# Kernel tuning notes

Measured on AMD Instinct MI355X. Metric: run time of the kernel, lower is better.

The kernel has to match this reference:

```python
import jax, jax.numpy as jnp
import numpy as np

B, L, D = 32, 8192, 256
M = L // 2 + 1  # max possible valley count (strict local minima can't be adjacent)


def setup_inputs() -> dict:
    key = jax.random.key(0)
    k1, k2, k3 = jax.random.split(key, 3)
    xs_pad = jax.random.normal(k1, (B, L, D), dtype=jnp.float32)
    olens = jax.random.randint(k2, (B,), 1, L + 1, dtype=jnp.int32)
    # linear_sigmoid params: Linear(256, 1)
    W = jax.random.normal(k3, (D, 1), dtype=jnp.float32) * 0.05
    b = jnp.zeros((1,), dtype=jnp.float32)
    return {"xs_pad": xs_pad, "olens": olens, "W": W, "b": b}


def reference(xs_pad, olens, W, b):
    Bq, Lq, Dq = xs_pad.shape
    # scalar importance: sigmoid(Linear(x))  [B, L, 1]
    s = jax.nn.sigmoid(xs_pad @ W + b)
    alpha_h = s * xs_pad                       # [B, L, D]
    sq = s[..., 0]                             # [B, L]
    # shifted neighbors, zero-padded at the ends (matches F.pad of the detached scalars)
    s_before = jnp.pad(sq[:, :-1], ((0, 0), (1, 0)))
    s_after = jnp.pad(sq[:, 1:], ((0, 0), (0, 1)))
    mask = (sq < s_before) & (sq < s_after)    # strict local minima
    mask = mask.at[:, 0].set(True)             # first frame forced to be a valley start
    counts = mask.sum(axis=1).astype(jnp.int32)  # per-batch valley count (returned olens)

    # valley starts, sorted, padded with sentinel L  -> [B, M]
    pos = jnp.arange(Lq)
    starts = jnp.sort(jnp.where(mask, pos, Lq), axis=1)[:, :M]
    valid = (starts < Lq)
    # segment = [start, min(start+2, L)) i.e. frames start and start+1 (clipped)
    i0 = jnp.clip(starts, 0, Lq - 1)
    i1 = jnp.clip(starts + 1, 0, Lq - 1)
    w0 = valid.astype(xs_pad.dtype)[..., None]
    w1 = ((starts + 1 < Lq) & valid).astype(xs_pad.dtype)[..., None]

    def gather(a, idx):
        return jnp.take_along_axis(a, idx[:, :, None], axis=1)

    num = gather(alpha_h, i0) * w0 + gather(alpha_h, i1) * w1   # [B, M, D]
    den = gather(s, i0) * w0 + gather(s, i1) * w1               # [B, M, 1]
    out = num / jnp.maximum(den, 1e-6)
    return out, counts
```

## Files before the change

### kernel.cpp

```cpp
#include <hip/hip_runtime.h>
#include <math.h>

#define B_ 32
#define L_ 8192
#define D_ 256
#define M_ 4097

__global__ __launch_bounds__(256) void k_sigmoid_dot(
    const float* __restrict__ x, const float* __restrict__ W,
    const float* __restrict__ bias, float* __restrict__ s)
{
    int row  = (blockIdx.x << 2) + (threadIdx.x >> 6);
    int lane = threadIdx.x & 63;
    const float4 xv = ((const float4*)(x + (size_t)row * D_))[lane];
    const float4 wv = ((const float4*)W)[lane];
    float p = xv.x * wv.x + xv.y * wv.y + xv.z * wv.z + xv.w * wv.w;
#pragma unroll
    for (int off = 32; off > 0; off >>= 1)
        p += __shfl_xor(p, off, 64);
    if (lane == 0) {
        float z = p + bias[0];
        s[row] = 1.0f / (1.0f + expf(-z));
    }
}

__global__ __launch_bounds__(256) void k_scan(
    const float* __restrict__ s, int* __restrict__ starts,
    int* __restrict__ counts, float* __restrict__ out_counts)
{
    int b = blockIdx.x;
    const float* sb = s + (size_t)b * L_;
    int t    = threadIdx.x;
    int base = t * 32;

    unsigned bits = 0;
    int cnt = 0;
    float sprev = (base == 0) ? 0.0f : sb[base - 1];
    float sc    = sb[base];
#pragma unroll 1
    for (int i = 0; i < 32; i++) {
        int l = base + i;
        float snext = (l == L_ - 1) ? 0.0f : sb[l + 1];
        bool m = (l == 0) ? true : ((sc < sprev) && (sc < snext));
        if (m) { bits |= (1u << i); cnt++; }
        sprev = sc;
        sc    = snext;
    }

    __shared__ int sh[256];
    sh[t] = cnt;
    __syncthreads();
    for (int off = 1; off < 256; off <<= 1) {
        int v = (t >= off) ? sh[t - off] : 0;
        __syncthreads();
        sh[t] += v;
        __syncthreads();
    }
    int excl  = sh[t] - cnt;
    int total = sh[255];

    int k = excl;
    for (int i = 0; i < 32; i++) {
        if (bits & (1u << i)) { starts[b * M_ + k] = base + i; k++; }
    }
    if (t == 0) {
        counts[b]     = total;
        out_counts[b] = (float)total;
    }
}

__global__ __launch_bounds__(64) void k_write(
    const float* __restrict__ x, const float* __restrict__ s,
    const int* __restrict__ starts, const int* __restrict__ counts,
    float* __restrict__ out)
{
    int k    = blockIdx.x;
    int b    = blockIdx.y;
    int lane = threadIdx.x;
    float4* orow = (float4*)(out + ((size_t)b * M_ + k) * D_);
    if (k >= counts[b]) {
        orow[lane] = make_float4(0.f, 0.f, 0.f, 0.f);
        return;
    }
    int p = starts[b * M_ + k];
    const float* sb = s + (size_t)b * L_;
    float s0 = sb[p];
    bool has1 = (p + 1 < L_);
    float s1 = has1 ? sb[p + 1] : 0.0f;
    float inv = 1.0f / fmaxf(s0 + s1, 1e-6f);

    const float4* x0 = (const float4*)(x + ((size_t)b * L_ + p) * D_);
    float4 a = x0[lane];
    float4 r;
    r.x = s0 * a.x; r.y = s0 * a.y; r.z = s0 * a.z; r.w = s0 * a.w;
    if (has1) {
        float4 c = (x0 + (D_ / 4))[lane];
        r.x += s1 * c.x; r.y += s1 * c.y; r.z += s1 * c.z; r.w += s1 * c.w;
    }
    r.x *= inv; r.y *= inv; r.z *= inv; r.w *= inv;
    orow[lane] = r;
}

extern "C" void kernel_launch(void* const* d_in, const int* in_sizes, int n_in,
                              void* d_out, int out_size, void* d_ws, size_t ws_size,
                              hipStream_t stream) {
    const float* x    = (const float*)d_in[0];
    const float* W    = (const float*)d_in[2];
    const float* bias = (const float*)d_in[3];

    float* out        = (float*)d_out;
    float* out_counts = out + (size_t)B_ * M_ * D_;

    float* s      = (float*)d_ws;
    int*   starts = (int*)((char*)d_ws + (size_t)B_ * L_ * 4);
    int*   counts = (int*)((char*)starts + (size_t)B_ * M_ * 4);

    k_sigmoid_dot<<<(B_ * L_) / 4, 256, 0, stream>>>(x, W, bias, s);
    k_scan<<<B_, 256, 0, stream>>>(s, starts, counts, out_counts);
    k_write<<<dim3(M_, B_), 64, 0, stream>>>(x, s, starts, counts, out);
}
```

Baseline: 422.5 us.

## Precompute valley weights in scan and widen write kernel blocks

The scan kernel now loads its 32-frame chunk with vectorized float4 reads, replaces the shared-memory block scan with a wave shuffle scan plus per-wave sums, and emits per-valley records holding the normalized weights and position. The write kernel reads one record per row instead of gathering s twice and dividing. It also processes 8 rows per 256-thread block instead of one row per 64-thread block, which cuts the launch grid size. The second x row load is now unconditional, using a clamped pointer. The workspace grows because records are float4 instead of int.

```diff
diff --git a/kernel.cpp b/kernel.cpp
--- a/kernel.cpp
+++ b/kernel.cpp
@@ -25,43 +25,71 @@
 }
 
 __global__ __launch_bounds__(256) void k_scan(
-    const float* __restrict__ s, int* __restrict__ starts,
+    const float* __restrict__ s, float4* __restrict__ rec,
     int* __restrict__ counts, float* __restrict__ out_counts)
 {
     int b = blockIdx.x;
     const float* sb = s + (size_t)b * L_;
     int t    = threadIdx.x;
+    int wid  = t >> 6;
+    int lane = t & 63;
     int base = t * 32;
+
+    float vals[34];
+    vals[0]  = (base == 0) ? 0.0f : sb[base - 1];
+    const float4* sb4 = (const float4*)(sb + base);
+#pragma unroll
+    for (int j = 0; j < 8; j++) {
+        float4 q = sb4[j];
+        vals[1 + 4 * j] = q.x; vals[2 + 4 * j] = q.y;
+        vals[3 + 4 * j] = q.z; vals[4 + 4 * j] = q.w;
+    }
+    vals[33] = (base + 32 >= L_) ? 0.0f : sb[base + 32];
 
     unsigned bits = 0;
     int cnt = 0;
-    float sprev = (base == 0) ? 0.0f : sb[base - 1];
-    float sc    = sb[base];
-#pragma unroll 1
+#pragma unroll
     for (int i = 0; i < 32; i++) {
-        int l = base + i;
-        float snext = (l == L_ - 1) ? 0.0f : sb[l + 1];
-        bool m = (l == 0) ? true : ((sc < sprev) && (sc < snext));
+        bool m = (base + i == 0)
+                 ? true
+                 : ((vals[i + 1] < vals[i]) && (vals[i + 1] < vals[i + 2]));
         if (m) { bits |= (1u << i); cnt++; }
-        sprev = sc;
-        sc    = snext;
     }
 
-    __shared__ int sh[256];
-    sh[t] = cnt;
+    int v = cnt;
+#pragma unroll
+    for (int off = 1; off < 64; off <<= 1) {
+        int u = __shfl_up(v, off, 64);
+        if (lane >= off) v += u;
+    }
+    __shared__ int wsum[4];
+    if (lane == 63) wsum[wid] = v;
     __syncthreads();
-    for (int off = 1; off < 256; off <<= 1) {
-        int v = (t >= off) ? sh[t - off] : 0;
-        __syncthreads();
-        sh[t] += v;
-        __syncthreads();
-    }
-    int excl  = sh[t] - cnt;
-    int total = sh[255];
+    int wo = 0;
+#pragma unroll
+    for (int w = 0; w < 4; w++)
+        if (w < wid) wo += wsum[w];
+    int excl  = v + wo - cnt;
+    int total = wsum[0] + wsum[1] + wsum[2] + wsum[3];
 
     int k = excl;
+#pragma unroll
     for (int i = 0; i < 32; i++) {
-        if (bits & (1u << i)) { starts[b * M_ + k] = base + i; k++; }
+        if (bits & (1u << i)) {
+            if (k < M_) {
+                int   p  = base + i;
+                float s0 = vals[i + 1];
+                float s1 = vals[i + 2];
+                float inv = 1.0f / fmaxf(s0 + s1, 1e-6f);
+                float4 r;
+                r.x = s0 * inv;
+                r.y = s1 * inv;
+                r.z = __int_as_float(p);
+                r.w = 0.0f;
+                rec[(size_t)b * M_ + k] = r;
+            }
+            k++;
+        }
     }
     if (t == 0) {
         counts[b]     = total;
@@ -69,36 +97,40 @@
     }
 }
 
-__global__ __launch_bounds__(64) void k_write(
-    const float* __restrict__ x, const float* __restrict__ s,
-    const int* __restrict__ starts, const int* __restrict__ counts,
-    float* __restrict__ out)
+__global__ __launch_bounds__(256) void k_write(
+    const float* __restrict__ x, const float4* __restrict__ rec,
+    const int* __restrict__ counts, float* __restrict__ out)
 {
-    int k    = blockIdx.x;
     int b    = blockIdx.y;
-    int lane = threadIdx.x;
-    float4* orow = (float4*)(out + ((size_t)b * M_ + k) * D_);
-    if (k >= counts[b]) {
-        orow[lane] = make_float4(0.f, 0.f, 0.f, 0.f);
-        return;
+    int wid  = threadIdx.x >> 6;
+    int lane = threadIdx.x & 63;
+    int cnt  = counts[b];
+    if (cnt > M_) cnt = M_;
+    int kb   = blockIdx.x * 8 + wid;
+#pragma unroll
+    for (int rr = 0; rr < 2; rr++) {
+        int k = kb + (rr << 2);
+        if (k >= M_) continue;
+        float4* orow = (float4*)(out + ((size_t)b * M_ + k) * D_);
+        if (k >= cnt) {
+            orow[lane] = make_float4(0.f, 0.f, 0.f, 0.f);
+            continue;
+        }
+        float4 r4 = rec[(size_t)b * M_ + k];
+        int p = __float_as_int(r4.z);
+        if (p < 0) p = 0;
+        if (p > L_ - 1) p = L_ - 1;
+        const float4* xp = (const float4*)(x + ((size_t)b * L_ + p) * D_);
+        float4 a = xp[lane];
+        const float4* xq = xp + ((p + 1 < L_) ? (D_ / 4) : 0);
+        float4 c = xq[lane];
+        float4 r;
+        r.x = r4.x * a.x + r4.y * c.x;
+        r.y = r4.x * a.y + r4.y * c.y;
+        r.z = r4.x * a.z + r4.y * c.z;
+        r.w = r4.x * a.w + r4.y * c.w;
+        orow[lane] = r;
     }
-    int p = starts[b * M_ + k];
-    const float* sb = s + (size_t)b * L_;
-    float s0 = sb[p];
-    bool has1 = (p + 1 < L_);
-    float s1 = has1 ? sb[p + 1] : 0.0f;
-    float inv = 1.0f / fmaxf(s0 + s1, 1e-6f);
-
-    const float4* x0 = (const float4*)(x + ((size_t)b * L_ + p) * D_);
-    float4 a = x0[lane];
-    float4 r;
-    r.x = s0 * a.x; r.y = s0 * a.y; r.z = s0 * a.z; r.w = s0 * a.w;
-    if (has1) {
-        float4 c = (x0 + (D_ / 4))[lane];
-        r.x += s1 * c.x; r.y += s1 * c.y; r.z += s1 * c.z; r.w += s1 * c.w;
-    }
-    r.x *= inv; r.y *= inv; r.z *= inv; r.w *= inv;
-    orow[lane] = r;
 }
 
 extern "C" void kernel_launch(void* const* d_in, const int* in_sizes, int n_in,
@@ -111,11 +143,11 @@
     float* out        = (float*)d_out;
     float* out_counts = out + (size_t)B_ * M_ * D_;
 
-    float* s      = (float*)d_ws;
-    int*   starts = (int*)((char*)d_ws + (size_t)B_ * L_ * 4);
-    int*   counts = (int*)((char*)starts + (size_t)B_ * M_ * 4);
+    float*  s      = (float*)d_ws;
+    float4* rec    = (float4*)((char*)d_ws + (size_t)B_ * L_ * 4);
+    int*    counts = (int*)((char*)rec + (size_t)B_ * M_ * 16);
 
     k_sigmoid_dot<<<(B_ * L_) / 4, 256, 0, stream>>>(x, W, bias, s);
-    k_scan<<<B_, 256, 0, stream>>>(s, starts, counts, out_counts);
-    k_write<<<dim3(M_, B_), 64, 0, stream>>>(x, s, starts, counts, out);
+    k_scan<<<B_, 256, 0, stream>>>(s, rec, counts, out_counts);
+    k_write<<<dim3((M_ + 7) / 8, B_), 256, 0, stream>>>(x, rec, counts, out);
 }
```

Result: no change. 419.7 us (-0.7%).
